# Kernel optimization log

Hardware: AMD Instinct MI355X
Metric: run time of the kernel (lower is better)

The kernel has to match this reference:

```python
import jax, jax.numpy as jnp
import numpy as np

B, L, D = 2, 2048, 2048
H, G, HD = 16, 4, 128
EPS = 1e-6
THETA_BASE = 10000.0


def setup_inputs() -> dict:
    key = jax.random.key(0)
    ks = jax.random.split(key, 5)
    x = jax.random.normal(ks[0], (B, L, D), jnp.float32)
    Wq = jax.random.normal(ks[1], (D, H * HD), jnp.float32) * 0.02
    Wk = jax.random.normal(ks[2], (D, G * HD), jnp.float32) * 0.02
    Wv = jax.random.normal(ks[3], (D, G * HD), jnp.float32) * 0.02
    Wo = jax.random.normal(ks[4], (H * HD, D), jnp.float32) * 0.02
    q_scale = jnp.ones((HD,), jnp.float32)
    k_scale = jnp.ones((HD,), jnp.float32)
    # Well-formed RoPE tables of shape [L, HD] (duplicated-half layout expected by apply_rope)
    inv_freq = 1.0 / (THETA_BASE ** (jnp.arange(0, HD // 2, dtype=jnp.float32) * 2.0 / HD))  # [HD/2]
    angles = jnp.arange(L, dtype=jnp.float32)[:, None] * inv_freq[None, :]  # [L, HD/2]
    angles = jnp.concatenate([angles, angles], axis=1)  # [L, HD]
    cos = jnp.cos(angles)
    sin = jnp.sin(angles)
    # Causal mask: True = masked (matches masked_fill(mask, -inf))
    mask = jnp.triu(jnp.ones((L, L), dtype=bool), k=1)
    return {"x": x, "Wq": Wq, "Wk": Wk, "Wv": Wv, "Wo": Wo,
            "q_scale": q_scale, "k_scale": k_scale, "cos": cos, "sin": sin, "mask": mask}


def _rmsnorm(x, scale):
    var = jnp.mean(x * x, axis=-1, keepdims=True)
    return x * jax.lax.rsqrt(var + EPS) * scale


def _rope(x, cos, sin):
    # x: [B, h, L, HD]; cos/sin: [L, HD]
    hd = x.shape[-1]
    x1, x2 = x[..., : hd // 2], x[..., hd // 2 :]
    rotated = jnp.concatenate([-x2, x1], axis=-1)
    return x * cos[None, None] + rotated * sin[None, None]


def reference(x, Wq, Wk, Wv, Wo, q_scale, k_scale, cos, sin, mask):
    b, l, _ = x.shape
    q = (x @ Wq).reshape(b, l, H, HD).transpose(0, 2, 1, 3)  # [B,H,L,HD]
    k = (x @ Wk).reshape(b, l, G, HD).transpose(0, 2, 1, 3)  # [B,G,L,HD]
    v = (x @ Wv).reshape(b, l, G, HD).transpose(0, 2, 1, 3)
    q = _rmsnorm(q, q_scale)
    k = _rmsnorm(k, k_scale)
    q = _rope(q, cos, sin)
    k = _rope(k, cos, sin)
    gs = H // G
    k = jnp.repeat(k, gs, axis=1)  # [B,H,L,HD]
    v = jnp.repeat(v, gs, axis=1)
    scores = jnp.einsum('bhqd,bhkd->bhqk', q, k)
    scores = jnp.where(mask, -jnp.inf, scores)
    # NB: faithful to the source's unusual scaling by head_dim**2 (not sqrt)
    w = jax.nn.softmax(scores / float(HD ** 2), axis=-1)
    out = jnp.einsum('bhqk,bhkd->bhqd', w, v).transpose(0, 2, 1, 3).reshape(b, l, H * HD)
    return out @ Wo
```

## Files before the change

kernel.cpp:

```cpp
#include <hip/hip_runtime.h>
#include <math.h>

#define SEQ 2048
#define DMODEL 2048
#define NHQ 16
#define NHK 4

typedef __attribute__((ext_vector_type(8))) short short8;
typedef __attribute__((ext_vector_type(4))) float floatx4;

__device__ __forceinline__ unsigned short f2bf(float f) {
  unsigned int u = __builtin_bit_cast(unsigned int, f);
  u += 0x7fffu + ((u >> 16) & 1u);
  return (unsigned short)(u >> 16);
}
__device__ __forceinline__ float bf2f(unsigned short s) {
  unsigned int u = ((unsigned int)s) << 16;
  return __builtin_bit_cast(float, u);
}

__global__ __launch_bounds__(256) void cast_bf16(const float* __restrict__ in,
                                                 unsigned short* __restrict__ out) {
  const size_t i = ((size_t)blockIdx.x * 256 + threadIdx.x) * 4;
  const float4 v = *(const float4*)(in + i);
  ushort4 w;
  w.x = f2bf(v.x); w.y = f2bf(v.y); w.z = f2bf(v.z); w.w = f2bf(v.w);
  *(ushort4*)(out + i) = w;
}

__global__ __launch_bounds__(256) void transpose_cast(const float* __restrict__ in,
                                                      unsigned short* __restrict__ out,
                                                      int R, int C) {
  __shared__ float tile[32][33];
  const int tx = threadIdx.x, ty = threadIdx.y;
  const int c0 = blockIdx.x * 32, r0 = blockIdx.y * 32;
#pragma unroll
  for (int j = 0; j < 4; ++j)
    tile[ty + j * 8][tx] = in[(size_t)(r0 + ty + j * 8) * C + c0 + tx];
  __syncthreads();
#pragma unroll
  for (int j = 0; j < 4; ++j)
    out[(size_t)(c0 + ty + j * 8) * R + r0 + tx] = f2bf(tile[tx][ty + j * 8]);
}

__global__ __launch_bounds__(256) void transpose_v(const unsigned short* __restrict__ in,
                                                   unsigned short* __restrict__ out) {
  __shared__ unsigned short tile[32][34];
  const int tx = threadIdx.x, ty = threadIdx.y;
  const int l0 = blockIdx.x * 32, d0 = blockIdx.y * 32;
  const int bg = blockIdx.z;
  const int b = bg >> 2, g = bg & 3;
#pragma unroll
  for (int j = 0; j < 4; ++j)
    tile[ty + j * 8][tx] = in[(size_t)(b * SEQ + l0 + ty + j * 8) * 3072 + 2560 + g * 128 + d0 + tx];
  __syncthreads();
#pragma unroll
  for (int j = 0; j < 4; ++j)
    out[((size_t)bg * 128 + d0 + ty + j * 8) * SEQ + l0 + tx] = tile[tx][ty + j * 8];
}

template <typename OutT>
__global__ __launch_bounds__(256) void gemm_bf16(const unsigned short* __restrict__ A,
                                                 const unsigned short* __restrict__ Bt,
                                                 OutT* __restrict__ C,
                                                 int M, int N, int K) {
  __shared__ unsigned short As[128 * 32];
  __shared__ unsigned short Bs[128 * 32];
  const int tid = threadIdx.x;
  const int wave = tid >> 6;
  const int lane = tid & 63;
  const int bm = blockIdx.y * 128;
  const int bn = blockIdx.x * 128;
  const int wr = wave >> 1;
  const int wc = wave & 1;
  const int m15 = lane & 15;
  const int quad = lane >> 4;

  floatx4 acc[4][4];
#pragma unroll
  for (int i = 0; i < 4; ++i)
#pragma unroll
    for (int j = 0; j < 4; ++j) acc[i][j] = (floatx4){0.f, 0.f, 0.f, 0.f};

  const int srow = lane >> 2;
  const int scol = (lane & 3) * 8;

  for (int k0 = 0; k0 < K; k0 += 32) {
#pragma unroll
    for (int it = 0; it < 2; ++it) {
      const int rowa = wave * 32 + it * 16;
      const unsigned short* ga = A + (size_t)(bm + rowa + srow) * K + k0 + scol;
      const unsigned short* gb = Bt + (size_t)(bn + rowa + srow) * K + k0 + scol;
      __builtin_amdgcn_global_load_lds(
          (const __attribute__((address_space(1))) void*)ga,
          (__attribute__((address_space(3))) void*)&As[rowa * 32], 16, 0, 0);
      __builtin_amdgcn_global_load_lds(
          (const __attribute__((address_space(1))) void*)gb,
          (__attribute__((address_space(3))) void*)&Bs[rowa * 32], 16, 0, 0);
    }
    __syncthreads();

    short8 af[4], bfr[4];
    const unsigned short* pa = &As[(wr * 64 + m15) * 32 + quad * 8];
    const unsigned short* pb = &Bs[(wc * 64 + m15) * 32 + quad * 8];
#pragma unroll
    for (int i = 0; i < 4; ++i) af[i] = *(const short8*)(pa + i * 16 * 32);
#pragma unroll
    for (int j = 0; j < 4; ++j) bfr[j] = *(const short8*)(pb + j * 16 * 32);
#pragma unroll
    for (int i = 0; i < 4; ++i)
#pragma unroll
      for (int j = 0; j < 4; ++j)
        acc[i][j] = __builtin_amdgcn_mfma_f32_16x16x32_bf16(af[i], bfr[j], acc[i][j], 0, 0, 0);
    __syncthreads();
  }

#pragma unroll
  for (int i = 0; i < 4; ++i)
#pragma unroll
    for (int j = 0; j < 4; ++j) {
      const int col = bn + wc * 64 + j * 16 + m15;
#pragma unroll
      for (int reg = 0; reg < 4; ++reg) {
        const int row = bm + wr * 64 + i * 16 + quad * 4 + reg;
        if constexpr (sizeof(OutT) == 2)
          C[(size_t)row * N + col] = f2bf(acc[i][j][reg]);
        else
          C[(size_t)row * N + col] = acc[i][j][reg];
      }
    }
}

__global__ __launch_bounds__(256) void rmsnorm_rope_qk(const unsigned short* __restrict__ qkv,
                                                       unsigned short* __restrict__ qout,
                                                       unsigned short* __restrict__ kout,
                                                       const float* __restrict__ q_scale,
                                                       const float* __restrict__ k_scale,
                                                       const float* __restrict__ cosb,
                                                       const float* __restrict__ sinb) {
  const int t = threadIdx.x;
  const int head = blockIdx.y * 4 + threadIdx.y;
  const int row = blockIdx.x;
  const int b = row >> 11;
  const int l = row & (SEQ - 1);
  const bool is_q = head < NHQ;
  const int colOff = is_q ? head * 128 : 2048 + (head - NHQ) * 128;
  const float* scale = is_q ? q_scale : k_scale;
  unsigned short* dst = is_q
      ? qout + ((size_t)(b * NHQ + head) * SEQ + l) * 128
      : kout + ((size_t)(b * NHK + (head - NHQ)) * SEQ + l) * 128;

  const unsigned short* base = qkv + (size_t)row * 3072 + colOff;
  const float v0 = bf2f(base[t]);
  const float v1 = bf2f(base[t + 64]);
  float ss = v0 * v0 + v1 * v1;
#pragma unroll
  for (int m = 1; m < 64; m <<= 1) ss += __shfl_xor(ss, m);
  const float r = rsqrtf(ss * (1.0f / 128.0f) + 1e-6f);
  const float a0 = v0 * r * scale[t];
  const float a1 = v1 * r * scale[t + 64];
  const float c0 = cosb[(size_t)l * 128 + t];
  const float s0 = sinb[(size_t)l * 128 + t];
  const float c1 = cosb[(size_t)l * 128 + t + 64];
  const float s1 = sinb[(size_t)l * 128 + t + 64];
  dst[t]      = f2bf(a0 * c0 - a1 * s0);
  dst[t + 64] = f2bf(a1 * c1 + a0 * s1);
}

__global__ __launch_bounds__(256, 3) void attn_mfma(const unsigned short* __restrict__ qb,
                                                    const unsigned short* __restrict__ kb,
                                                    const unsigned short* __restrict__ vtb,
                                                    unsigned short* __restrict__ o) {
  __shared__ unsigned short Ks[64 * 128];
  __shared__ unsigned short Vs[128 * 64];
  __shared__ unsigned short Ps[64 * 72];

  const int tid = threadIdx.x;
  const int wave = tid >> 6;
  const int lane = tid & 63;
  const int m15 = lane & 15;
  const int quad = lane >> 4;
  const int bh = blockIdx.x;
  const int b = bh >> 4;
  const int h = bh & 15;
  const int g = h >> 2;
  const int q0 = ((int)gridDim.y - 1 - (int)blockIdx.y) * 64;

  const unsigned short* qhead = qb + (size_t)bh * SEQ * 128;
  const unsigned short* khead = kb + (size_t)(b * NHK + g) * SEQ * 128;
  const unsigned short* vthead = vtb + (size_t)(b * NHK + g) * 128 * SEQ;

  short8 qf[4];
  {
    const unsigned short* qp = qhead + (size_t)(q0 + wave * 16 + m15) * 128 + quad * 8;
#pragma unroll
    for (int ks = 0; ks < 4; ++ks) qf[ks] = *(const short8*)(qp + ks * 32);
  }

  floatx4 acc_o[8];
#pragma unroll
  for (int n = 0; n < 8; ++n) acc_o[n] = (floatx4){0.f, 0.f, 0.f, 0.f};
  float l_lane[4] = {0.f, 0.f, 0.f, 0.f};
  const float inv_scale = 1.0f / 16384.0f;

  for (int j0 = 0; j0 <= q0; j0 += 64) {
#pragma unroll
    for (int t = 0; t < 4; ++t) {
      const int r = wave * 16 + t * 4 + (lane >> 4);
      const int cg = (lane & 15) ^ (r & 15);
      const unsigned short* src = khead + (size_t)(j0 + r) * 128 + cg * 8;
      __builtin_amdgcn_global_load_lds(
          (const __attribute__((address_space(1))) void*)src,
          (__attribute__((address_space(3))) void*)&Ks[(wave * 16 + t * 4) * 128], 16, 0, 0);
    }
#pragma unroll
    for (int t = 0; t < 4; ++t) {
      const int d = wave * 32 + t * 8 + (lane >> 3);
      const int cg = (lane & 7) ^ (d & 7);
      const unsigned short* src = vthead + (size_t)d * SEQ + j0 + cg * 8;
      __builtin_amdgcn_global_load_lds(
          (const __attribute__((address_space(1))) void*)src,
          (__attribute__((address_space(3))) void*)&Vs[(wave * 32 + t * 8) * 64], 16, 0, 0);
    }
    __syncthreads();

    floatx4 acc_s[4];
#pragma unroll
    for (int n = 0; n < 4; ++n) acc_s[n] = (floatx4){0.f, 0.f, 0.f, 0.f};
#pragma unroll
    for (int ks = 0; ks < 4; ++ks) {
#pragma unroll
      for (int n = 0; n < 4; ++n) {
        const short8 bfrag = *(const short8*)&Ks[(n * 16 + m15) * 128 + (((ks * 4 + quad) ^ m15) * 8)];
        acc_s[n] = __builtin_amdgcn_mfma_f32_16x16x32_bf16(qf[ks], bfrag, acc_s[n], 0, 0, 0);
      }
    }

    if (j0 == q0) {
      const int row_g = wave * 16 + quad * 4;
#pragma unroll
      for (int n = 0; n < 4; ++n) {
        const int col = n * 16 + m15;
#pragma unroll
        for (int rg = 0; rg < 4; ++rg) {
          float p = (col > row_g + rg) ? 0.0f : __expf(acc_s[n][rg] * inv_scale);
          l_lane[rg] += p;
          Ps[(wave * 16 + quad * 4 + rg) * 72 + n * 16 + m15] = f2bf(p);
        }
      }
    } else {
#pragma unroll
      for (int n = 0; n < 4; ++n) {
#pragma unroll
        for (int rg = 0; rg < 4; ++rg) {
          const float p = __expf(acc_s[n][rg] * inv_scale);
          l_lane[rg] += p;
          Ps[(wave * 16 + quad * 4 + rg) * 72 + n * 16 + m15] = f2bf(p);
        }
      }
    }

#pragma unroll
    for (int kk = 0; kk < 2; ++kk) {
      const short8 a = *(const short8*)&Ps[(wave * 16 + m15) * 72 + kk * 32 + quad * 8];
#pragma unroll
      for (int n = 0; n < 8; ++n) {
        const short8 bfrag = *(const short8*)&Vs[(n * 16 + m15) * 64 + (((kk * 4 + quad) ^ (m15 & 7)) * 8)];
        acc_o[n] = __builtin_amdgcn_mfma_f32_16x16x32_bf16(a, bfrag, acc_o[n], 0, 0, 0);
      }
    }
    __syncthreads();
  }

#pragma unroll
  for (int rg = 0; rg < 4; ++rg) {
    float l = l_lane[rg];
    l += __shfl_xor(l, 1);
    l += __shfl_xor(l, 2);
    l += __shfl_xor(l, 4);
    l += __shfl_xor(l, 8);
    const float invl = 1.0f / l;
    const size_t row = (size_t)(b * SEQ + q0 + wave * 16 + quad * 4 + rg);
#pragma unroll
    for (int n = 0; n < 8; ++n)
      o[row * DMODEL + h * 128 + n * 16 + m15] = f2bf(acc_o[n][rg] * invl);
  }
}

extern "C" void kernel_launch(void* const* d_in, const int* in_sizes, int n_in,
                              void* d_out, int out_size, void* d_ws, size_t ws_size,
                              hipStream_t stream) {
  const float* x       = (const float*)d_in[0];
  const float* Wq      = (const float*)d_in[1];
  const float* Wk      = (const float*)d_in[2];
  const float* Wv      = (const float*)d_in[3];
  const float* Wo      = (const float*)d_in[4];
  const float* q_scale = (const float*)d_in[5];
  const float* k_scale = (const float*)d_in[6];
  const float* cosb    = (const float*)d_in[7];
  const float* sinb    = (const float*)d_in[8];
  float* out = (float*)d_out;

  char* w = (char*)d_ws;
  unsigned short* x_bf   = (unsigned short*)w;
  unsigned short* qkv_bf = (unsigned short*)(w + 16777216);
  unsigned short* wqkv_t = (unsigned short*)(w + 41943040);
  unsigned short* k_bf   = (unsigned short*)(w + 54525952);
  unsigned short* vt     = (unsigned short*)(w + 58720256);
  unsigned short* wo_t   = (unsigned short*)(w + 62914560);
  unsigned short* q_bf    = (unsigned short*)w;
  unsigned short* attn_bf = (unsigned short*)(w + 16777216);

  cast_bf16<<<(4096 * 2048 / 4) / 256, 256, 0, stream>>>(x, x_bf);
  transpose_cast<<<dim3(2048 / 32, 2048 / 32), dim3(32, 8), 0, stream>>>(Wq, wqkv_t, 2048, 2048);
  transpose_cast<<<dim3(512 / 32, 2048 / 32), dim3(32, 8), 0, stream>>>(Wk, wqkv_t + (size_t)2048 * 2048, 2048, 512);
  transpose_cast<<<dim3(512 / 32, 2048 / 32), dim3(32, 8), 0, stream>>>(Wv, wqkv_t + (size_t)2560 * 2048, 2048, 512);
  transpose_cast<<<dim3(2048 / 32, 2048 / 32), dim3(32, 8), 0, stream>>>(Wo, wo_t, 2048, 2048);

  gemm_bf16<unsigned short><<<dim3(3072 / 128, 4096 / 128), 256, 0, stream>>>(
      x_bf, wqkv_t, qkv_bf, 4096, 3072, 2048);

  rmsnorm_rope_qk<<<dim3(4096, 5), dim3(64, 4), 0, stream>>>(qkv_bf, q_bf, k_bf,
                                                             q_scale, k_scale, cosb, sinb);
  transpose_v<<<dim3(SEQ / 32, 128 / 32, 2 * NHK), dim3(32, 8), 0, stream>>>(qkv_bf, vt);

  attn_mfma<<<dim3(2 * NHQ, SEQ / 64), 256, 0, stream>>>(q_bf, k_bf, vt, attn_bf);
  gemm_bf16<float><<<dim3(2048 / 128, 4096 / 128), 256, 0, stream>>>(
      attn_bf, wo_t, out, 4096, 2048, 2048);
}
```

Before: 341.8 us.

## Fuse RMSNorm, RoPE and V transpose into QKV GEMM epilogue; merge weight transposes

The QKV GEMM now stages its 128x128 output tile in shared memory and applies RMSNorm plus RoPE for Q/K heads, or writes V transposed, directly in the epilogue. This removes the intermediate qkv buffer round trip and two separate kernel launches. The four weight-transpose launches are merged into one launch indexed by blockIdx.z, and workspace offsets are reorganised to match. The epilogue adds serial per-row shuffle reductions and a larger shared-memory footprint, which may lower occupancy of the GEMM.

```diff
diff --git a/kernel.cpp b/kernel.cpp
--- a/kernel.cpp
+++ b/kernel.cpp
@@ -28,12 +28,28 @@
   *(ushort4*)(out + i) = w;
 }
 
-__global__ __launch_bounds__(256) void transpose_cast(const float* __restrict__ in,
-                                                      unsigned short* __restrict__ out,
-                                                      int R, int C) {
+__global__ __launch_bounds__(256) void transpose_weights(const float* __restrict__ Wq,
+                                                         const float* __restrict__ Wk,
+                                                         const float* __restrict__ Wv,
+                                                         const float* __restrict__ Wo,
+                                                         unsigned short* __restrict__ wqkv_t,
+                                                         unsigned short* __restrict__ wo_t) {
+  const int z = blockIdx.z;
+  int bx = blockIdx.x;
+  const float* in;
+  unsigned short* out;
+  int C;
+  const int R = 2048;
+  if (z == 0)      { in = Wq; out = wqkv_t;                         C = 2048; }
+  else if (z == 1) { in = Wo; out = wo_t;                           C = 2048; }
+  else {
+    if (bx < 16)      { in = Wk; out = wqkv_t + (size_t)2048 * 2048; C = 512; }
+    else if (bx < 32) { in = Wv; out = wqkv_t + (size_t)2560 * 2048; C = 512; bx -= 16; }
+    else return;
+  }
   __shared__ float tile[32][33];
   const int tx = threadIdx.x, ty = threadIdx.y;
-  const int c0 = blockIdx.x * 32, r0 = blockIdx.y * 32;
+  const int c0 = bx * 32, r0 = blockIdx.y * 32;
 #pragma unroll
   for (int j = 0; j < 4; ++j)
     tile[ty + j * 8][tx] = in[(size_t)(r0 + ty + j * 8) * C + c0 + tx];
@@ -43,27 +59,131 @@
     out[(size_t)(c0 + ty + j * 8) * R + r0 + tx] = f2bf(tile[tx][ty + j * 8]);
 }
 
-__global__ __launch_bounds__(256) void transpose_v(const unsigned short* __restrict__ in,
-                                                   unsigned short* __restrict__ out) {
-  __shared__ unsigned short tile[32][34];
-  const int tx = threadIdx.x, ty = threadIdx.y;
-  const int l0 = blockIdx.x * 32, d0 = blockIdx.y * 32;
-  const int bg = blockIdx.z;
-  const int b = bg >> 2, g = bg & 3;
-#pragma unroll
-  for (int j = 0; j < 4; ++j)
-    tile[ty + j * 8][tx] = in[(size_t)(b * SEQ + l0 + ty + j * 8) * 3072 + 2560 + g * 128 + d0 + tx];
+__global__ __launch_bounds__(256) void gemm_qkv_fused(const unsigned short* __restrict__ A,
+                                                      const unsigned short* __restrict__ Bt,
+                                                      unsigned short* __restrict__ qout,
+                                                      unsigned short* __restrict__ kout,
+                                                      unsigned short* __restrict__ vout,
+                                                      const float* __restrict__ q_scale,
+                                                      const float* __restrict__ k_scale,
+                                                      const float* __restrict__ cosb,
+                                                      const float* __restrict__ sinb) {
+  __shared__ unsigned short smem[128 * 129];
+  unsigned short* As = smem;
+  unsigned short* Bs = smem + 128 * 32;
+
+  const int tid = threadIdx.x;
+  const int wave = tid >> 6;
+  const int lane = tid & 63;
+  const int bm = blockIdx.y * 128;
+  const int bx = blockIdx.x;
+  const int bn = bx * 128;
+  const int wr = wave >> 1;
+  const int wc = wave & 1;
+  const int m15 = lane & 15;
+  const int quad = lane >> 4;
+
+  floatx4 acc[4][4];
+#pragma unroll
+  for (int i = 0; i < 4; ++i)
+#pragma unroll
+    for (int j = 0; j < 4; ++j) acc[i][j] = (floatx4){0.f, 0.f, 0.f, 0.f};
+
+  const int srow = lane >> 2;
+  const int scol = (lane & 3) * 8;
+
+  for (int k0 = 0; k0 < 2048; k0 += 32) {
+#pragma unroll
+    for (int it = 0; it < 2; ++it) {
+      const int rowa = wave * 32 + it * 16;
+      const unsigned short* ga = A + (size_t)(bm + rowa + srow) * 2048 + k0 + scol;
+      const unsigned short* gb = Bt + (size_t)(bn + rowa + srow) * 2048 + k0 + scol;
+      __builtin_amdgcn_global_load_lds(
+          (const __attribute__((address_space(1))) void*)ga,
+          (__attribute__((address_space(3))) void*)&As[rowa * 32], 16, 0, 0);
+      __builtin_amdgcn_global_load_lds(
+          (const __attribute__((address_space(1))) void*)gb,
+          (__attribute__((address_space(3))) void*)&Bs[rowa * 32], 16, 0, 0);
+    }
+    __syncthreads();
+
+    short8 af[4], bfr[4];
+    const unsigned short* pa = &As[(wr * 64 + m15) * 32 + quad * 8];
+    const unsigned short* pb = &Bs[(wc * 64 + m15) * 32 + quad * 8];
+#pragma unroll
+    for (int i = 0; i < 4; ++i) af[i] = *(const short8*)(pa + i * 16 * 32);
+#pragma unroll
+    for (int j = 0; j < 4; ++j) bfr[j] = *(const short8*)(pb + j * 16 * 32);
+#pragma unroll
+    for (int i = 0; i < 4; ++i)
+#pragma unroll
+      for (int j = 0; j < 4; ++j)
+        acc[i][j] = __builtin_amdgcn_mfma_f32_16x16x32_bf16(af[i], bfr[j], acc[i][j], 0, 0, 0);
+    __syncthreads();
+  }
+
+#pragma unroll
+  for (int i = 0; i < 4; ++i)
+#pragma unroll
+    for (int j = 0; j < 4; ++j) {
+      const int col = wc * 64 + j * 16 + m15;
+#pragma unroll
+      for (int reg = 0; reg < 4; ++reg) {
+        const int row = wr * 64 + i * 16 + quad * 4 + reg;
+        smem[row * 129 + col] = f2bf(acc[i][j][reg]);
+      }
+    }
   __syncthreads();
-#pragma unroll
-  for (int j = 0; j < 4; ++j)
-    out[((size_t)bg * 128 + d0 + ty + j * 8) * SEQ + l0 + tx] = tile[tx][ty + j * 8];
-}
-
-template <typename OutT>
-__global__ __launch_bounds__(256) void gemm_bf16(const unsigned short* __restrict__ A,
-                                                 const unsigned short* __restrict__ Bt,
-                                                 OutT* __restrict__ C,
-                                                 int M, int N, int K) {
+
+  const int t = tid & 63;
+  const int wv = tid >> 6;
+  const int b = bm >> 11;
+  const int l_base = bm & (SEQ - 1);
+
+  if (bx < 20) {
+    const float* scale = (bx < NHQ) ? q_scale : k_scale;
+    unsigned short* dstbase = (bx < NHQ)
+        ? qout + ((size_t)(b * NHQ + bx) * SEQ + l_base) * 128
+        : kout + ((size_t)(b * NHK + (bx - NHQ)) * SEQ + l_base) * 128;
+    const float sc0 = scale[t];
+    const float sc1 = scale[t + 64];
+#pragma unroll 4
+    for (int rr = 0; rr < 32; ++rr) {
+      const int row = wv * 32 + rr;
+      const float v0 = bf2f(smem[row * 129 + t]);
+      const float v1 = bf2f(smem[row * 129 + t + 64]);
+      float ss = v0 * v0 + v1 * v1;
+#pragma unroll
+      for (int m = 1; m < 64; m <<= 1) ss += __shfl_xor(ss, m);
+      const float r = rsqrtf(ss * (1.0f / 128.0f) + 1e-6f);
+      const int l = l_base + row;
+      const float c0 = cosb[(size_t)l * 128 + t];
+      const float s0 = sinb[(size_t)l * 128 + t];
+      const float c1 = cosb[(size_t)l * 128 + t + 64];
+      const float s1 = sinb[(size_t)l * 128 + t + 64];
+      const float a0 = v0 * r * sc0;
+      const float a1 = v1 * r * sc1;
+      unsigned short* dst = dstbase + (size_t)row * 128;
+      dst[t]      = f2bf(a0 * c0 - a1 * s0);
+      dst[t + 64] = f2bf(a1 * c1 + a0 * s1);
+    }
+  } else {
+    const int g = bx - 20;
+    unsigned short* vbase = vout + (size_t)(b * NHK + g) * 128 * SEQ + l_base;
+#pragma unroll 4
+    for (int dd = 0; dd < 32; ++dd) {
+      const int d = wv * 32 + dd;
+      unsigned short* dst = vbase + (size_t)d * SEQ;
+      dst[t]      = smem[t * 129 + d];
+      dst[t + 64] = smem[(t + 64) * 129 + d];
+    }
+  }
+}
+
+__global__ __launch_bounds__(256) void gemm_bf16_f32(const unsigned short* __restrict__ A,
+                                                     const unsigned short* __restrict__ Bt,
+                                                     float* __restrict__ C,
+                                                     int M, int N, int K) {
   __shared__ unsigned short As[128 * 32];
   __shared__ unsigned short Bs[128 * 32];
   const int tid = threadIdx.x;
@@ -123,48 +243,9 @@
 #pragma unroll
       for (int reg = 0; reg < 4; ++reg) {
         const int row = bm + wr * 64 + i * 16 + quad * 4 + reg;
-        if constexpr (sizeof(OutT) == 2)
-          C[(size_t)row * N + col] = f2bf(acc[i][j][reg]);
-        else
-          C[(size_t)row * N + col] = acc[i][j][reg];
-      }
-    }
-}
-
-__global__ __launch_bounds__(256) void rmsnorm_rope_qk(const unsigned short* __restrict__ qkv,
-                                                       unsigned short* __restrict__ qout,
-                                                       unsigned short* __restrict__ kout,
-                                                       const float* __restrict__ q_scale,
-                                                       const float* __restrict__ k_scale,
-                                                       const float* __restrict__ cosb,
-                                                       const float* __restrict__ sinb) {
-  const int t = threadIdx.x;
-  const int head = blockIdx.y * 4 + threadIdx.y;
-  const int row = blockIdx.x;
-  const int b = row >> 11;
-  const int l = row & (SEQ - 1);
-  const bool is_q = head < NHQ;
-  const int colOff = is_q ? head * 128 : 2048 + (head - NHQ) * 128;
-  const float* scale = is_q ? q_scale : k_scale;
-  unsigned short* dst = is_q
-      ? qout + ((size_t)(b * NHQ + head) * SEQ + l) * 128
-      : kout + ((size_t)(b * NHK + (head - NHQ)) * SEQ + l) * 128;
-
-  const unsigned short* base = qkv + (size_t)row * 3072 + colOff;
-  const float v0 = bf2f(base[t]);
-  const float v1 = bf2f(base[t + 64]);
-  float ss = v0 * v0 + v1 * v1;
-#pragma unroll
-  for (int m = 1; m < 64; m <<= 1) ss += __shfl_xor(ss, m);
-  const float r = rsqrtf(ss * (1.0f / 128.0f) + 1e-6f);
-  const float a0 = v0 * r * scale[t];
-  const float a1 = v1 * r * scale[t + 64];
-  const float c0 = cosb[(size_t)l * 128 + t];
-  const float s0 = sinb[(size_t)l * 128 + t];
-  const float c1 = cosb[(size_t)l * 128 + t + 64];
-  const float s1 = sinb[(size_t)l * 128 + t + 64];
-  dst[t]      = f2bf(a0 * c0 - a1 * s0);
-  dst[t + 64] = f2bf(a1 * c1 + a0 * s1);
+        C[(size_t)row * N + col] = acc[i][j][reg];
+      }
+    }
 }
 
 __global__ __launch_bounds__(256, 3) void attn_mfma(const unsigned short* __restrict__ qb,
@@ -302,29 +383,21 @@
   float* out = (float*)d_out;
 
   char* w = (char*)d_ws;
-  unsigned short* x_bf   = (unsigned short*)w;
-  unsigned short* qkv_bf = (unsigned short*)(w + 16777216);
-  unsigned short* wqkv_t = (unsigned short*)(w + 41943040);
-  unsigned short* k_bf   = (unsigned short*)(w + 54525952);
-  unsigned short* vt     = (unsigned short*)(w + 58720256);
-  unsigned short* wo_t   = (unsigned short*)(w + 62914560);
-  unsigned short* q_bf    = (unsigned short*)w;
-  unsigned short* attn_bf = (unsigned short*)(w + 16777216);
+  unsigned short* x_bf    = (unsigned short*)w;
+  unsigned short* wqkv_t  = (unsigned short*)(w + 16777216);
+  unsigned short* q_bf    = (unsigned short*)(w + 29360128);
+  unsigned short* k_bf    = (unsigned short*)(w + 46137344);
+  unsigned short* vt      = (unsigned short*)(w + 50331648);
+  unsigned short* wo_t    = (unsigned short*)(w + 54525952);
+  unsigned short* attn_bf = (unsigned short*)(w + 62914560);
 
   cast_bf16<<<(4096 * 2048 / 4) / 256, 256, 0, stream>>>(x, x_bf);
-  transpose_cast<<<dim3(2048 / 32, 2048 / 32), dim3(32, 8), 0, stream>>>(Wq, wqkv_t, 2048, 2048);
-  transpose_cast<<<dim3(512 / 32, 2048 / 32), dim3(32, 8), 0, stream>>>(Wk, wqkv_t + (size_t)2048 * 2048, 2048, 512);
-  transpose_cast<<<dim3(512 / 32, 2048 / 32), dim3(32, 8), 0, stream>>>(Wv, wqkv_t + (size_t)2560 * 2048, 2048, 512);
-  transpose_cast<<<dim3(2048 / 32, 2048 / 32), dim3(32, 8), 0, stream>>>(Wo, wo_t, 2048, 2048);
-
-  gemm_bf16<unsigned short><<<dim3(3072 / 128, 4096 / 128), 256, 0, stream>>>(
-      x_bf, wqkv_t, qkv_bf, 4096, 3072, 2048);
-
-  rmsnorm_rope_qk<<<dim3(4096, 5), dim3(64, 4), 0, stream>>>(qkv_bf, q_bf, k_bf,
-                                                             q_scale, k_scale, cosb, sinb);
-  transpose_v<<<dim3(SEQ / 32, 128 / 32, 2 * NHK), dim3(32, 8), 0, stream>>>(qkv_bf, vt);
+  transpose_weights<<<dim3(64, 64, 3), dim3(32, 8), 0, stream>>>(Wq, Wk, Wv, Wo, wqkv_t, wo_t);
+
+  gemm_qkv_fused<<<dim3(24, 32), 256, 0, stream>>>(x_bf, wqkv_t, q_bf, k_bf, vt,
+                                                   q_scale, k_scale, cosb, sinb);
 
   attn_mfma<<<dim3(2 * NHQ, SEQ / 64), 256, 0, stream>>>(q_bf, k_bf, vt, attn_bf);
-  gemm_bf16<float><<<dim3(2048 / 128, 4096 / 128), 256, 0, stream>>>(
+  gemm_bf16_f32<<<dim3(2048 / 128, 4096 / 128), 256, 0, stream>>>(
       attn_bf, wo_t, out, 4096, 2048, 2048);
 }
```

Measured after the change: 327.6 us. 1.04x faster.
